# Kernel optimization log

Hardware: AMD Instinct MI355X
Metric: run time of the kernel (lower is better)

The kernel has to match this reference:

```python
import jax, jax.numpy as jnp
import numpy as np

EPS = 1e-5
NUM_HEADS = 12

def _ln(x, g, b):
    m = jnp.mean(x, -1, keepdims=True)
    v = jnp.var(x, -1, keepdims=True)
    return (x - m) * jax.lax.rsqrt(v + EPS) * g + b

def setup_inputs():
    key = jax.random.key(0)
    ks = jax.random.split(key, 8)
    D, Dh = 768, 3072
    B, T, H, Wd = 8, 8, 14, 14
    def w(k, shape, scale=0.02):
        return jax.random.normal(k, shape, jnp.float32) * scale
    return dict(
        x=jax.random.normal(ks[0], (B, T * H * Wd + 1, D), jnp.float32),
        W_mq=w(ks[1], (D, D)), b_mq=jnp.zeros((D,), jnp.float32),
        W_mk=w(ks[2], (D, D)), b_mk=jnp.zeros((D,), jnp.float32),
        g1=jnp.ones((D,), jnp.float32), be1=jnp.zeros((D,), jnp.float32),
        W_qkv=w(ks[3], (3 * D, D)),
        W_proj=w(ks[4], (D, D)), b_proj=jnp.zeros((D,), jnp.float32),
        g2=jnp.ones((D,), jnp.float32), be2=jnp.zeros((D,), jnp.float32),
        W_fc1=w(ks[5], (Dh, D)), b_fc1=jnp.zeros((Dh,), jnp.float32),
        W_fc2=w(ks[6], (D, Dh)), b_fc2=jnp.zeros((D,), jnp.float32),
        B=B, T=T, H=H, Wd=Wd,
    )

def reference(x, W_mq, b_mq, W_mk, b_mk, g1, be1, W_qkv, W_proj, b_proj,
              g2, be2, W_fc1, b_fc1, W_fc2, b_fc2, B, T, H, Wd):
    D = x.shape[-1]
    nh = NUM_HEADS
    hd = D // nh
    res = x
    # cls token: (B,1,D) -> repeated per frame -> (B*T,1,D)
    cls = jnp.repeat(x[:, :1, :], T, axis=1).reshape(B * T, 1, D)
    # spatial tokens: 'b (h w t) m -> (b t) (h w) m'  (t is fastest-varying)
    xs = x[:, 1:, :].reshape(B, H * Wd, T, D).transpose(0, 2, 1, 3).reshape(B * T, H * Wd, D)
    xt = jnp.concatenate([cls, xs], axis=1)  # (BT, N=197, D)
    # learned QK-gated mask
    qm = xt @ W_mq.T + b_mq
    km = xt @ W_mk.T + b_mk
    lm = jnp.einsum('bnd,bmd->bnm', qm, km)
    lm = lm.at[:, 0, 0].set(100.0)  # force cls->cls gate open
    lm = jax.nn.sigmoid(lm)
    # attention (drop rates are 0; drop_path is identity at inference)
    xn = _ln(xt, g1, be1)
    BT, N = xt.shape[0], xt.shape[1]
    qkv = (xn @ W_qkv.T).reshape(BT, N, 3, nh, hd).transpose(2, 0, 3, 1, 4)
    q, k, v = qkv[0], qkv[1], qkv[2]  # (BT, nh, N, hd)
    attn = jax.nn.softmax(jnp.einsum('bhnd,bhmd->bhnm', q, k) * (hd ** -0.5), axis=-1)
    attn = attn * lm[:, None, :, :]  # gate attention probs with learned mask
    o = jnp.einsum('bhnm,bhmd->bhnd', attn, v).transpose(0, 2, 1, 3).reshape(BT, N, D)
    o = o @ W_proj.T + b_proj
    # gather cls back (mean over frames) and scatter tokens back
    cls_o = jnp.mean(o[:, 0, :].reshape(B, T, D), axis=1, keepdims=True)  # (B,1,D)
    xs_o = o[:, 1:, :].reshape(B, T, H * Wd, D).transpose(0, 2, 1, 3).reshape(B, H * Wd * T, D)
    y = res + jnp.concatenate([cls_o, xs_o], axis=1)
    # MLP
    h = _ln(y, g2, be2)
    h = jax.nn.gelu(h @ W_fc1.T + b_fc1, approximate=False)
    y = y + (h @ W_fc2.T + b_fc2)
    return (y, lm)
```

## Files before the change

### kernel.cpp

```cpp
#include <hip/hip_runtime.h>
#include <cstdint>

typedef _Float16 f16;
typedef f16 f16x2 __attribute__((ext_vector_type(2)));
typedef f16 f16x4 __attribute__((ext_vector_type(4)));
typedef f16 f16x8 __attribute__((ext_vector_type(8)));
typedef float f32x4 __attribute__((ext_vector_type(4)));

constexpr int D = 768;
constexpr int NTOK = 197;
constexpr int BT = 64;
constexpr int ROWS_A = BT * NTOK;
constexpr int SEQ = 1569;
constexpr int ROWS_Y = 8 * SEQ;
constexpr int DH = 3072;
constexpr int CW = 2304;
constexpr long Y_ELEMS = (long)ROWS_Y * D;

__device__ __forceinline__ void gload_lds16(const f16* g, f16* l) {
  __builtin_amdgcn_global_load_lds(
      (const __attribute__((address_space(1))) void*)g,
      (__attribute__((address_space(3))) void*)l, 16, 0, 0);
}

__global__ __launch_bounds__(256) void cvt_f16(const float* __restrict__ in,
                                               f16* __restrict__ out, int n4) {
  int i = blockIdx.x * 256 + threadIdx.x;
  if (i >= n4) return;
  const float4 v = *(const float4*)(in + (size_t)i * 4);
  f16x4 o = {(f16)v.x, (f16)v.y, (f16)v.z, (f16)v.w};
  *(f16x4*)(out + (size_t)i * 4) = o;
}

__global__ __launch_bounds__(256) void concat2_f32(const float* __restrict__ a,
                                                   const float* __restrict__ b,
                                                   float* __restrict__ o, int n) {
  int i = blockIdx.x * 256 + threadIdx.x;
  if (i < n) o[i] = a[i];
  else if (i < 2 * n) o[i] = b[i - n];
}

__global__ __launch_bounds__(192) void build_xt_xn(
    const float* __restrict__ x, const float* __restrict__ g1,
    const float* __restrict__ be1, f16* __restrict__ xt, f16* __restrict__ xn) {
  const int rid = blockIdx.x;
  const int bt = rid / NTOK, n = rid % NTOK;
  const int b = bt >> 3, t = bt & 7;
  const int src = (n == 0) ? b * SEQ : b * SEQ + 1 + (n - 1) * 8 + t;
  const int tid = threadIdx.x, d0 = tid * 4;
  const float4 v = *(const float4*)(x + (size_t)src * D + d0);
  float s = v.x + v.y + v.z + v.w;
  float q = v.x * v.x + v.y * v.y + v.z * v.z + v.w * v.w;
  const int lane = tid & 63, wv = tid >> 6;
  for (int off = 32; off; off >>= 1) {
    s += __shfl_xor(s, off);
    q += __shfl_xor(q, off);
  }
  __shared__ float red[2][3];
  if (lane == 0) { red[0][wv] = s; red[1][wv] = q; }
  __syncthreads();
  s = red[0][0] + red[0][1] + red[0][2];
  q = red[1][0] + red[1][1] + red[1][2];
  const float mean = s * (1.f / 768.f);
  const float var = q * (1.f / 768.f) - mean * mean;
  const float rs = rsqrtf(var + 1e-5f);
  const size_t ob = (size_t)rid * D + d0;
  f16x4 xo = {(f16)v.x, (f16)v.y, (f16)v.z, (f16)v.w};
  *(f16x4*)(xt + ob) = xo;
  const float4 gv = *(const float4*)(g1 + d0);
  const float4 bv = *(const float4*)(be1 + d0);
  f16x4 no = {(f16)((v.x - mean) * rs * gv.x + bv.x),
              (f16)((v.y - mean) * rs * gv.y + bv.y),
              (f16)((v.z - mean) * rs * gv.z + bv.z),
              (f16)((v.w - mean) * rs * gv.w + bv.w)};
  *(f16x4*)(xn + ob) = no;
}

constexpr int EPI_F16 = 0;
constexpr int EPI_F16_BIAS = 1;
constexpr int EPI_SIG = 2;
constexpr int EPI_F16_BIAS_GELU = 3;
constexpr int EPI_F32_BIAS_RES = 4;

template <int EPI>
__global__ __launch_bounds__(256, 3) void gemm_f16(
    const f16* __restrict__ A, const f16* __restrict__ B,
    const float* __restrict__ bias, float* __restrict__ Cf,
    f16* __restrict__ Ch, const float* __restrict__ Res, int M, int N, int K,
    int lda, int ldb, int ldc, long sA, long sB, long sC) {
  constexpr int BM = 128, BN = 128, BK = 32;
  __shared__ f16 As[2][BM][BK];
  __shared__ f16 Bs[2][BN][BK];
  const int tid = threadIdx.x;
  const int bm = blockIdx.y * BM, bn = blockIdx.x * BN;
  const int z = blockIdx.z;
  A += (size_t)z * sA;
  B += (size_t)z * sB;
  const int lane = tid & 63, wave = tid >> 6;
  const int wm = (wave >> 1) * 64, wn = (wave & 1) * 64;
  const int l15 = lane & 15, quad = lane >> 4;

  const int gr = lane >> 2;
  const int gc = (lane & 3) * 8;
  int a_row0 = bm + wave * 16 + gr;       if (a_row0 >= M) a_row0 = M - 1;
  int a_row1 = bm + (wave + 4) * 16 + gr; if (a_row1 >= M) a_row1 = M - 1;
  int b_row0 = bn + wave * 16 + gr;       if (b_row0 >= N) b_row0 = N - 1;
  int b_row1 = bn + (wave + 4) * 16 + gr; if (b_row1 >= N) b_row1 = N - 1;
  const f16* ap0 = A + (size_t)a_row0 * lda + gc;
  const f16* ap1 = A + (size_t)a_row1 * lda + gc;
  const f16* bp0 = B + (size_t)b_row0 * ldb + gc;
  const f16* bp1 = B + (size_t)b_row1 * ldb + gc;

  f32x4 acc[4][4] = {};

  auto stage = [&](int buf, int k) {
    gload_lds16(ap0 + k, &As[buf][wave * 16][0]);
    gload_lds16(ap1 + k, &As[buf][(wave + 4) * 16][0]);
    gload_lds16(bp0 + k, &Bs[buf][wave * 16][0]);
    gload_lds16(bp1 + k, &Bs[buf][(wave + 4) * 16][0]);
  };
  auto compute = [&](int buf) {
    f16x8 af[4], bf[4];
#pragma unroll
    for (int i = 0; i < 4; i++) {
      af[i] = *(const f16x8*)&As[buf][wm + i * 16 + l15][quad * 8];
      bf[i] = *(const f16x8*)&Bs[buf][wn + i * 16 + l15][quad * 8];
    }
#pragma unroll
    for (int i = 0; i < 4; i++)
#pragma unroll
      for (int j = 0; j < 4; j++)
        acc[i][j] =
            __builtin_amdgcn_mfma_f32_16x16x32_f16(af[i], bf[j], acc[i][j], 0, 0, 0);
  };

  stage(0, 0);
  __syncthreads();
  for (int kt = 0; kt < K; kt += 2 * BK) {
    stage(1, kt + BK);
    compute(0);
    __syncthreads();
    if (kt + 2 * BK < K) stage(0, kt + 2 * BK);
    compute(1);
    __syncthreads();
  }

#pragma unroll
  for (int i = 0; i < 4; i++) {
#pragma unroll
    for (int j = 0; j < 4; j++) {
      const int col = bn + wn + j * 16 + l15;
      if (col >= N) continue;
#pragma unroll
      for (int r = 0; r < 4; r++) {
        const int row = bm + wm + i * 16 + quad * 4 + r;
        if (row >= M) continue;
        float v = acc[i][j][r];
        const size_t ci = (size_t)z * sC + (size_t)row * ldc + col;
        if constexpr (EPI == EPI_F16) {
          Ch[ci] = (f16)v;
        } else if constexpr (EPI == EPI_F16_BIAS) {
          Ch[ci] = (f16)(v + bias[col]);
        } else if constexpr (EPI == EPI_SIG) {
          if (row == 0 && col == 0) v = 100.f;
          Cf[ci] = 1.f / (1.f + __expf(-v));
        } else if constexpr (EPI == EPI_F16_BIAS_GELU) {
          const float u = v + bias[col];
          const float t = u * (0.79788456f + 0.0356774081f * u * u);
          const float e = __expf(2.f * t);
          Ch[ci] = (f16)(u * (e / (e + 1.f)));
        } else if constexpr (EPI == EPI_F32_BIAS_RES) {
          Cf[ci] = v + bias[col] + Res[ci];
        }
      }
    }
  }
}

__global__ __launch_bounds__(256, 2) void attn_kernel(
    const f16* __restrict__ qkv, const float* __restrict__ lm,
    f16* __restrict__ o) {
  __shared__ f16 Ks[208][72];
  __shared__ f16 Vt[64][232];
  __shared__ f16 Ps[4][16][40];
  const int bh = blockIdx.x;
  const int bt = bh / 12, h = bh % 12;
  const int tid = threadIdx.x, lane = tid & 63, w = tid >> 6;
  const int l15 = lane & 15, quad = lane >> 4;
  const size_t base = (size_t)bt * NTOK * CW + (size_t)h * 64;

  for (int idx = tid; idx < 208 * 8; idx += 256) {
    const int r = idx >> 3, c = (idx & 7) * 8;
    f16x8 kv = {};
    if (r < NTOK) kv = *(const f16x8*)(qkv + base + (size_t)r * CW + 768 + c);
    *(f16x8*)&Ks[r][c] = kv;
  }
  for (int cb = 0; cb < 8; cb++) {
    const int r = tid;
    if (r < NTOK) {
      const f16x8 vv = *(const f16x8*)(qkv + base + (size_t)r * CW + 1536 + cb * 8);
#pragma unroll
      for (int j = 0; j < 8; j++) Vt[cb * 8 + j][r] = vv[j];
    }
  }
  for (int idx = tid; idx < 64 * 35; idx += 256) {
    const int d = idx / 35, m = NTOK + idx % 35;
    Vt[d][m] = (f16)0.f;
  }
  __syncthreads();

  for (int nt = w; nt < 13; nt += 4) {
    const int nq = nt * 16 + l15;
    const f16* qrow = qkv + base + (size_t)nq * CW;
    const f16x8 aq0 = *(const f16x8*)(qrow + quad * 8);
    const f16x8 aq1 = *(const f16x8*)(qrow + 32 + quad * 8);
    f32x4 S[13];
#pragma unroll
    for (int t = 0; t < 13; t++) {
      const f16x8 bk0 = *(const f16x8*)&Ks[t * 16 + l15][quad * 8];
      const f16x8 bk1 = *(const f16x8*)&Ks[t * 16 + l15][32 + quad * 8];
      f32x4 s = {};
      s = __builtin_amdgcn_mfma_f32_16x16x32_f16(aq0, bk0, s, 0, 0, 0);
      s = __builtin_amdgcn_mfma_f32_16x16x32_f16(aq1, bk1, s, 0, 0, 0);
      S[t] = s;
    }
    float mx[4] = {-3e38f, -3e38f, -3e38f, -3e38f};
#pragma unroll
    for (int t = 0; t < 13; t++) {
      const int m = t * 16 + l15;
#pragma unroll
      for (int r = 0; r < 4; r++) {
        float v = (m < NTOK) ? S[t][r] * 0.125f : -1e30f;
        S[t][r] = v;
        mx[r] = fmaxf(mx[r], v);
      }
    }
#pragma unroll
    for (int off = 1; off < 16; off <<= 1)
#pragma unroll
      for (int r = 0; r < 4; r++) mx[r] = fmaxf(mx[r], __shfl_xor(mx[r], off));
    float den[4] = {0.f, 0.f, 0.f, 0.f};
#pragma unroll
    for (int t = 0; t < 13; t++)
#pragma unroll
      for (int r = 0; r < 4; r++) {
        const float e = __expf(S[t][r] - mx[r]);
        S[t][r] = e;
        den[r] += e;
      }
#pragma unroll
    for (int off = 1; off < 16; off <<= 1)
#pragma unroll
      for (int r = 0; r < 4; r++) den[r] += __shfl_xor(den[r], off);
    float inv[4];
#pragma unroll
    for (int r = 0; r < 4; r++) inv[r] = 1.f / den[r];
#pragma unroll
    for (int t = 0; t < 13; t++) {
      const int m = t * 16 + l15;
#pragma unroll
      for (int r = 0; r < 4; r++) {
        const int nrow = nt * 16 + quad * 4 + r;
        float g = 0.f;
        if (m < NTOK && nrow < NTOK)
          g = lm[((size_t)bt * NTOK + nrow) * NTOK + m];
        S[t][r] *= inv[r] * g;
      }
    }
    f32x4 O[4] = {};
    for (int c = 0; c < 7; c++) {
      __builtin_amdgcn_wave_barrier();
#pragma unroll
      for (int tt = 0; tt < 2; tt++) {
        const int t = 2 * c + tt;
#pragma unroll
        for (int r = 0; r < 4; r++) {
          const f16 pv = (t < 13) ? (f16)S[t][r] : (f16)0.f;
          Ps[w][quad * 4 + r][tt * 16 + l15] = pv;
        }
      }
      __builtin_amdgcn_wave_barrier();
      const f16x8 ap = *(const f16x8*)&Ps[w][l15][quad * 8];
#pragma unroll
      for (int dt = 0; dt < 4; dt++) {
        const f16x8 bv = *(const f16x8*)&Vt[dt * 16 + l15][c * 32 + quad * 8];
        O[dt] = __builtin_amdgcn_mfma_f32_16x16x32_f16(ap, bv, O[dt], 0, 0, 0);
      }
    }
#pragma unroll
    for (int dt = 0; dt < 4; dt++)
#pragma unroll
      for (int r = 0; r < 4; r++) {
        const int nrow = nt * 16 + quad * 4 + r;
        if (nrow < NTOK)
          o[((size_t)bt * NTOK + nrow) * D + h * 64 + dt * 16 + l15] =
              (f16)O[dt][r];
      }
  }
}

__global__ __launch_bounds__(192) void scatter_y_ln(
    const float* __restrict__ x, const f16* __restrict__ po,
    const float* __restrict__ g2, const float* __restrict__ be2,
    float* __restrict__ y, f16* __restrict__ yn) {
  const int rid = blockIdx.x;
  const int b = rid / SEQ, pos = rid % SEQ;
  const int tid = threadIdx.x, d0 = tid * 4;
  float4 v = *(const float4*)(x + (size_t)rid * D + d0);
  if (pos == 0) {
    float ax = 0, ay = 0, az = 0, aw = 0;
    for (int t = 0; t < 8; t++) {
      const f16x4 p = *(const f16x4*)(po + ((size_t)(b * 8 + t) * NTOK) * D + d0);
      ax += (float)p[0]; ay += (float)p[1]; az += (float)p[2]; aw += (float)p[3];
    }
    v.x += ax * 0.125f; v.y += ay * 0.125f; v.z += az * 0.125f; v.w += aw * 0.125f;
  } else {
    const int hw = (pos - 1) >> 3, t = (pos - 1) & 7;
    const f16x4 p =
        *(const f16x4*)(po + ((size_t)((b * 8 + t) * NTOK + 1 + hw)) * D + d0);
    v.x += (float)p[0]; v.y += (float)p[1]; v.z += (float)p[2]; v.w += (float)p[3];
  }
  *(float4*)(y + (size_t)rid * D + d0) = v;
  float s = v.x + v.y + v.z + v.w;
  float q = v.x * v.x + v.y * v.y + v.z * v.z + v.w * v.w;
  const int lane = tid & 63, wv = tid >> 6;
  for (int off = 32; off; off >>= 1) {
    s += __shfl_xor(s, off);
    q += __shfl_xor(q, off);
  }
  __shared__ float red[2][3];
  if (lane == 0) { red[0][wv] = s; red[1][wv] = q; }
  __syncthreads();
  s = red[0][0] + red[0][1] + red[0][2];
  q = red[1][0] + red[1][1] + red[1][2];
  const float mean = s * (1.f / 768.f);
  const float var = q * (1.f / 768.f) - mean * mean;
  const float rs = rsqrtf(var + 1e-5f);
  const float4 gv = *(const float4*)(g2 + d0);
  const float4 bv = *(const float4*)(be2 + d0);
  f16x4 no = {(f16)((v.x - mean) * rs * gv.x + bv.x),
              (f16)((v.y - mean) * rs * gv.y + bv.y),
              (f16)((v.z - mean) * rs * gv.z + bv.z),
              (f16)((v.w - mean) * rs * gv.w + bv.w)};
  *(f16x4*)(yn + (size_t)rid * D + d0) = no;
}

extern "C" void kernel_launch(void* const* d_in, const int* in_sizes, int n_in,
                              void* d_out, int out_size, void* d_ws,
                              size_t ws_size, hipStream_t stream) {
  const float* x = (const float*)d_in[0];
  const float* W_mq = (const float*)d_in[1];
  const float* b_mq = (const float*)d_in[2];
  const float* W_mk = (const float*)d_in[3];
  const float* b_mk = (const float*)d_in[4];
  const float* g1 = (const float*)d_in[5];
  const float* be1 = (const float*)d_in[6];
  const float* W_qkv = (const float*)d_in[7];
  const float* W_proj = (const float*)d_in[8];
  const float* b_proj = (const float*)d_in[9];
  const float* g2 = (const float*)d_in[10];
  const float* be2 = (const float*)d_in[11];
  const float* W_fc1 = (const float*)d_in[12];
  const float* b_fc1 = (const float*)d_in[13];
  const float* W_fc2 = (const float*)d_in[14];
  const float* b_fc2 = (const float*)d_in[15];

  char* ws = (char*)d_ws;
  size_t off = 0;
  auto alloc = [&](size_t bytes) {
    size_t o = off;
    off = (off + bytes + 255) & ~(size_t)255;
    return o;
  };
  const size_t o_wmqk = alloc((size_t)2 * D * D * 2);
  const size_t o_bmqk = alloc((size_t)2 * D * 4);
  const size_t o_wqkv = alloc((size_t)CW * D * 2);
  const size_t o_wproj = alloc((size_t)D * D * 2);
  const size_t o_wfc1 = alloc((size_t)DH * D * 2);
  const size_t o_wfc2 = alloc((size_t)D * DH * 2);
  const size_t o_xt = alloc((size_t)ROWS_A * D * 2);
  const size_t o_xn = alloc((size_t)ROWS_A * D * 2);
  const size_t o_big = alloc((size_t)ROWS_A * CW * 2);
  const size_t o_po = alloc((size_t)ROWS_A * D * 2);
  const size_t o_qmkm = o_big;
  const size_t o_qkv = o_big;
  const size_t o_o = o_xn;
  const size_t o_yn = o_xt;
  const size_t o_h = o_big;

  f16* wmqk = (f16*)(ws + o_wmqk);
  float* bmqk = (float*)(ws + o_bmqk);
  f16* wqkv = (f16*)(ws + o_wqkv);
  f16* wproj = (f16*)(ws + o_wproj);
  f16* wfc1 = (f16*)(ws + o_wfc1);
  f16* wfc2 = (f16*)(ws + o_wfc2);
  f16* xt = (f16*)(ws + o_xt);
  f16* xn = (f16*)(ws + o_xn);
  f16* qmkm = (f16*)(ws + o_qmkm);
  f16* qkv = (f16*)(ws + o_qkv);
  f16* oatt = (f16*)(ws + o_o);
  f16* po = (f16*)(ws + o_po);
  f16* yn = (f16*)(ws + o_yn);
  f16* h = (f16*)(ws + o_h);

  float* y_out = (float*)d_out;
  float* lm_out = (float*)d_out + Y_ELEMS;

  const dim3 blk(256);
  auto cvt = [&](const float* src, f16* dst, int n) {
    cvt_f16<<<dim3((n / 4 + 255) / 256), blk, 0, stream>>>(src, dst, n / 4);
  };
  cvt(W_mq, wmqk, D * D);
  cvt(W_mk, wmqk + (size_t)D * D, D * D);
  cvt(W_qkv, wqkv, CW * D);
  cvt(W_proj, wproj, D * D);
  cvt(W_fc1, wfc1, DH * D);
  cvt(W_fc2, wfc2, D * DH);
  concat2_f32<<<dim3(6), blk, 0, stream>>>(b_mq, b_mk, bmqk, D);

  build_xt_xn<<<dim3(ROWS_A), dim3(192), 0, stream>>>(x, g1, be1, xt, xn);

  auto grd = [](int N_, int M_, int Z_) {
    return dim3((N_ + 127) / 128, (M_ + 127) / 128, Z_);
  };
  gemm_f16<EPI_F16_BIAS><<<grd(2 * D, ROWS_A, 1), blk, 0, stream>>>(
      xt, wmqk, bmqk, nullptr, qmkm, nullptr, ROWS_A, 2 * D, D, D, D, 2 * D,
      0, 0, 0);
  gemm_f16<EPI_SIG><<<grd(NTOK, NTOK, BT), blk, 0, stream>>>(
      qmkm, qmkm + D, nullptr, lm_out, nullptr, nullptr, NTOK, NTOK, D,
      2 * D, 2 * D, NTOK, (long)NTOK * 2 * D, (long)NTOK * 2 * D,
      (long)NTOK * NTOK);
  gemm_f16<EPI_F16><<<grd(CW, ROWS_A, 1), blk, 0, stream>>>(
      xn, wqkv, nullptr, nullptr, qkv, nullptr, ROWS_A, CW, D, D, D, CW,
      0, 0, 0);
  attn_kernel<<<dim3(BT * 12), blk, 0, stream>>>(qkv, lm_out, oatt);
  gemm_f16<EPI_F16_BIAS><<<grd(D, ROWS_A, 1), blk, 0, stream>>>(
      oatt, wproj, b_proj, nullptr, po, nullptr, ROWS_A, D, D, D, D, D,
      0, 0, 0);
  scatter_y_ln<<<dim3(ROWS_Y), dim3(192), 0, stream>>>(x, po, g2, be2, y_out, yn);
  gemm_f16<EPI_F16_BIAS_GELU><<<grd(DH, ROWS_Y, 1), blk, 0, stream>>>(
      yn, wfc1, b_fc1, nullptr, h, nullptr, ROWS_Y, DH, D, D, D, DH, 0, 0, 0);
  gemm_f16<EPI_F32_BIAS_RES><<<grd(D, ROWS_Y, 1), blk, 0, stream>>>(
      h, wfc2, b_fc2, y_out, nullptr, y_out, ROWS_Y, D, DH, DH, DH, D,
      0, 0, 0);
  (void)in_sizes; (void)n_in; (void)out_size; (void)ws_size;
}
```

Baseline: 666.4 us.

## Triple-buffer GEMM K loop, split-K FC2 with atomics, fuse weight conversions

The GEMM main loop moves from two LDS buffers with two barriers per pair of K tiles to three buffers with one barrier per K tile. A vmcnt wait lets the loads two tiles ahead stay in flight while the current tile is computed. FC2 now runs as a 2-way split-K with atomicAdd into y, which doubles its grid. The fc2 bias is folded into the residual write in scatter_y_ln so the atomic epilogue only adds partial sums. The six weight conversion launches are merged into one. The extra LDS (24KB per block) may lower occupancy, and atomics make the FC2 summation order nondeterministic.

```diff
diff --git a/kernel.cpp b/kernel.cpp
--- a/kernel.cpp
+++ b/kernel.cpp
@@ -23,13 +23,31 @@
       (__attribute__((address_space(3))) void*)l, 16, 0, 0);
 }
 
-__global__ __launch_bounds__(256) void cvt_f16(const float* __restrict__ in,
-                                               f16* __restrict__ out, int n4) {
-  int i = blockIdx.x * 256 + threadIdx.x;
-  if (i >= n4) return;
-  const float4 v = *(const float4*)(in + (size_t)i * 4);
+constexpr int DD4 = D * D / 4;
+constexpr int QKV4 = CW * D / 4;
+constexpr int FC4 = DH * D / 4;
+constexpr int WQ_TOT = 3 * DD4 + QKV4 + 2 * FC4;
+
+__global__ __launch_bounds__(256) void cvt_weights(
+    const float* __restrict__ wmq_f, const float* __restrict__ wmk_f,
+    const float* __restrict__ wqkv_f, const float* __restrict__ wproj_f,
+    const float* __restrict__ wfc1_f, const float* __restrict__ wfc2_f,
+    f16* __restrict__ wmqk, f16* __restrict__ wqkv, f16* __restrict__ wproj,
+    f16* __restrict__ wfc1, f16* __restrict__ wfc2) {
+  const int i = blockIdx.x * 256 + threadIdx.x;
+  const float* src;
+  f16* dst;
+  int j;
+  if (i < DD4) { src = wmq_f; dst = wmqk; j = i; }
+  else if (i < 2 * DD4) { src = wmk_f; dst = wmqk + (size_t)D * D; j = i - DD4; }
+  else if (i < 2 * DD4 + QKV4) { src = wqkv_f; dst = wqkv; j = i - 2 * DD4; }
+  else if (i < 3 * DD4 + QKV4) { src = wproj_f; dst = wproj; j = i - 2 * DD4 - QKV4; }
+  else if (i < 3 * DD4 + QKV4 + FC4) { src = wfc1_f; dst = wfc1; j = i - 3 * DD4 - QKV4; }
+  else if (i < WQ_TOT) { src = wfc2_f; dst = wfc2; j = i - 3 * DD4 - QKV4 - FC4; }
+  else return;
+  const float4 v = *(const float4*)(src + (size_t)j * 4);
   f16x4 o = {(f16)v.x, (f16)v.y, (f16)v.z, (f16)v.w};
-  *(f16x4*)(out + (size_t)i * 4) = o;
+  *(f16x4*)(dst + (size_t)j * 4) = o;
 }
 
 __global__ __launch_bounds__(256) void concat2_f32(const float* __restrict__ a,
@@ -81,6 +99,7 @@
 constexpr int EPI_SIG = 2;
 constexpr int EPI_F16_BIAS_GELU = 3;
 constexpr int EPI_F32_BIAS_RES = 4;
+constexpr int EPI_F32_ATOMIC = 5;
 
 template <int EPI>
 __global__ __launch_bounds__(256, 3) void gemm_f16(
@@ -89,8 +108,8 @@
     f16* __restrict__ Ch, const float* __restrict__ Res, int M, int N, int K,
     int lda, int ldb, int ldc, long sA, long sB, long sC) {
   constexpr int BM = 128, BN = 128, BK = 32;
-  __shared__ f16 As[2][BM][BK];
-  __shared__ f16 Bs[2][BN][BK];
+  __shared__ f16 As[3][BM][BK];
+  __shared__ f16 Bs[3][BN][BK];
   const int tid = threadIdx.x;
   const int bm = blockIdx.y * BM, bn = blockIdx.x * BN;
   const int z = blockIdx.z;
@@ -134,16 +153,22 @@
             __builtin_amdgcn_mfma_f32_16x16x32_f16(af[i], bf[j], acc[i][j], 0, 0, 0);
   };
 
+  const int NT = K / BK;
   stage(0, 0);
-  __syncthreads();
-  for (int kt = 0; kt < K; kt += 2 * BK) {
-    stage(1, kt + BK);
-    compute(0);
-    __syncthreads();
-    if (kt + 2 * BK < K) stage(0, kt + 2 * BK);
-    compute(1);
-    __syncthreads();
-  }
+  stage(1, BK);
+  for (int kt = 0; kt < NT - 1; ++kt) {
+    asm volatile("s_waitcnt vmcnt(4)" ::: "memory");
+    __builtin_amdgcn_sched_barrier(0);
+    __builtin_amdgcn_s_barrier();
+    __builtin_amdgcn_sched_barrier(0);
+    if (kt + 2 < NT) stage((kt + 2) % 3, (kt + 2) * BK);
+    compute(kt % 3);
+  }
+  asm volatile("s_waitcnt vmcnt(0)" ::: "memory");
+  __builtin_amdgcn_sched_barrier(0);
+  __builtin_amdgcn_s_barrier();
+  __builtin_amdgcn_sched_barrier(0);
+  compute((NT - 1) % 3);
 
 #pragma unroll
   for (int i = 0; i < 4; i++) {
@@ -171,6 +196,8 @@
           Ch[ci] = (f16)(u * (e / (e + 1.f)));
         } else if constexpr (EPI == EPI_F32_BIAS_RES) {
           Cf[ci] = v + bias[col] + Res[ci];
+        } else if constexpr (EPI == EPI_F32_ATOMIC) {
+          atomicAdd(Cf + ci, v);
         }
       }
     }
@@ -302,6 +329,7 @@
 __global__ __launch_bounds__(192) void scatter_y_ln(
     const float* __restrict__ x, const f16* __restrict__ po,
     const float* __restrict__ g2, const float* __restrict__ be2,
+    const float* __restrict__ bfc2,
     float* __restrict__ y, f16* __restrict__ yn) {
   const int rid = blockIdx.x;
   const int b = rid / SEQ, pos = rid % SEQ;
@@ -320,7 +348,9 @@
         *(const f16x4*)(po + ((size_t)((b * 8 + t) * NTOK + 1 + hw)) * D + d0);
     v.x += (float)p[0]; v.y += (float)p[1]; v.z += (float)p[2]; v.w += (float)p[3];
   }
-  *(float4*)(y + (size_t)rid * D + d0) = v;
+  const float4 b2 = *(const float4*)(bfc2 + d0);
+  float4 vo = {v.x + b2.x, v.y + b2.y, v.z + b2.z, v.w + b2.w};
+  *(float4*)(y + (size_t)rid * D + d0) = vo;
   float s = v.x + v.y + v.z + v.w;
   float q = v.x * v.x + v.y * v.y + v.z * v.z + v.w * v.w;
   const int lane = tid & 63, wv = tid >> 6;
@@ -407,15 +437,8 @@
   float* lm_out = (float*)d_out + Y_ELEMS;
 
   const dim3 blk(256);
-  auto cvt = [&](const float* src, f16* dst, int n) {
-    cvt_f16<<<dim3((n / 4 + 255) / 256), blk, 0, stream>>>(src, dst, n / 4);
-  };
-  cvt(W_mq, wmqk, D * D);
-  cvt(W_mk, wmqk + (size_t)D * D, D * D);
-  cvt(W_qkv, wqkv, CW * D);
-  cvt(W_proj, wproj, D * D);
-  cvt(W_fc1, wfc1, DH * D);
-  cvt(W_fc2, wfc2, D * DH);
+  cvt_weights<<<dim3((WQ_TOT + 255) / 256), blk, 0, stream>>>(
+      W_mq, W_mk, W_qkv, W_proj, W_fc1, W_fc2, wmqk, wqkv, wproj, wfc1, wfc2);
   concat2_f32<<<dim3(6), blk, 0, stream>>>(b_mq, b_mk, bmqk, D);
 
   build_xt_xn<<<dim3(ROWS_A), dim3(192), 0, stream>>>(x, g1, be1, xt, xn);
@@ -437,11 +460,12 @@
   gemm_f16<EPI_F16_BIAS><<<grd(D, ROWS_A, 1), blk, 0, stream>>>(
       oatt, wproj, b_proj, nullptr, po, nullptr, ROWS_A, D, D, D, D, D,
       0, 0, 0);
-  scatter_y_ln<<<dim3(ROWS_Y), dim3(192), 0, stream>>>(x, po, g2, be2, y_out, yn);
+  scatter_y_ln<<<dim3(ROWS_Y), dim3(192), 0, stream>>>(x, po, g2, be2, b_fc2,
+                                                       y_out, yn);
   gemm_f16<EPI_F16_BIAS_GELU><<<grd(DH, ROWS_Y, 1), blk, 0, stream>>>(
       yn, wfc1, b_fc1, nullptr, h, nullptr, ROWS_Y, DH, D, D, D, DH, 0, 0, 0);
-  gemm_f16<EPI_F32_BIAS_RES><<<grd(D, ROWS_Y, 1), blk, 0, stream>>>(
-      h, wfc2, b_fc2, y_out, nullptr, y_out, ROWS_Y, D, DH, DH, DH, D,
-      0, 0, 0);
+  gemm_f16<EPI_F32_ATOMIC><<<grd(D, ROWS_Y, 2), blk, 0, stream>>>(
+      h, wfc2, nullptr, y_out, nullptr, nullptr, ROWS_Y, D, 1536, DH, DH, D,
+      1536, 1536, 0);
   (void)in_sizes; (void)n_in; (void)out_size; (void)ws_size;
 }
```

Measured after the change: 677.1 us. About the same (+1.6%).

## Merge weight conversions into one launch and use 128x64 tiles for N=768 GEMMs

Applied to the files above, without the earlier changes.

Replaces six separate fp32-to-fp16 weight conversion launches with a single kernel that selects source and destination by index range, cutting launch overhead. The GEMM is templated on N-tile width and occupancy. The proj and fc2 GEMMs (N=768) now use 128x64 tiles with launch bounds allowing 4 blocks per CU, doubling block count so the 256 CUs are filled better. The trade-off is lower per-block arithmetic intensity and more A-tile reloads for those GEMMs.

```diff
diff --git a/kernel.cpp b/kernel.cpp
--- a/kernel.cpp
+++ b/kernel.cpp
@@ -23,13 +23,31 @@
       (__attribute__((address_space(3))) void*)l, 16, 0, 0);
 }
 
-__global__ __launch_bounds__(256) void cvt_f16(const float* __restrict__ in,
-                                               f16* __restrict__ out, int n4) {
-  int i = blockIdx.x * 256 + threadIdx.x;
-  if (i >= n4) return;
-  const float4 v = *(const float4*)(in + (size_t)i * 4);
+constexpr int DD4 = D * D / 4;
+constexpr int QKV4 = CW * D / 4;
+constexpr int FC4 = DH * D / 4;
+constexpr int WQ_TOT = 3 * DD4 + QKV4 + 2 * FC4;
+
+__global__ __launch_bounds__(256) void cvt_weights(
+    const float* __restrict__ wmq_f, const float* __restrict__ wmk_f,
+    const float* __restrict__ wqkv_f, const float* __restrict__ wproj_f,
+    const float* __restrict__ wfc1_f, const float* __restrict__ wfc2_f,
+    f16* __restrict__ wmqk, f16* __restrict__ wqkv, f16* __restrict__ wproj,
+    f16* __restrict__ wfc1, f16* __restrict__ wfc2) {
+  const int i = blockIdx.x * 256 + threadIdx.x;
+  const float* src;
+  f16* dst;
+  int j;
+  if (i < DD4) { src = wmq_f; dst = wmqk; j = i; }
+  else if (i < 2 * DD4) { src = wmk_f; dst = wmqk + (size_t)D * D; j = i - DD4; }
+  else if (i < 2 * DD4 + QKV4) { src = wqkv_f; dst = wqkv; j = i - 2 * DD4; }
+  else if (i < 3 * DD4 + QKV4) { src = wproj_f; dst = wproj; j = i - 2 * DD4 - QKV4; }
+  else if (i < 3 * DD4 + QKV4 + FC4) { src = wfc1_f; dst = wfc1; j = i - 3 * DD4 - QKV4; }
+  else if (i < WQ_TOT) { src = wfc2_f; dst = wfc2; j = i - 3 * DD4 - QKV4 - FC4; }
+  else return;
+  const float4 v = *(const float4*)(src + (size_t)j * 4);
   f16x4 o = {(f16)v.x, (f16)v.y, (f16)v.z, (f16)v.w};
-  *(f16x4*)(out + (size_t)i * 4) = o;
+  *(f16x4*)(dst + (size_t)j * 4) = o;
 }
 
 __global__ __launch_bounds__(256) void concat2_f32(const float* __restrict__ a,
@@ -82,22 +100,23 @@
 constexpr int EPI_F16_BIAS_GELU = 3;
 constexpr int EPI_F32_BIAS_RES = 4;
 
-template <int EPI>
-__global__ __launch_bounds__(256, 3) void gemm_f16(
+template <int EPI, int BNT = 128, int WPE = 3>
+__global__ __launch_bounds__(256, WPE) void gemm_f16(
     const f16* __restrict__ A, const f16* __restrict__ B,
     const float* __restrict__ bias, float* __restrict__ Cf,
     f16* __restrict__ Ch, const float* __restrict__ Res, int M, int N, int K,
     int lda, int ldb, int ldc, long sA, long sB, long sC) {
-  constexpr int BM = 128, BN = 128, BK = 32;
+  constexpr int BM = 128, BK = 32;
+  constexpr int NJ = BNT / 32;
   __shared__ f16 As[2][BM][BK];
-  __shared__ f16 Bs[2][BN][BK];
+  __shared__ f16 Bs[2][BNT][BK];
   const int tid = threadIdx.x;
-  const int bm = blockIdx.y * BM, bn = blockIdx.x * BN;
+  const int bm = blockIdx.y * BM, bn = blockIdx.x * BNT;
   const int z = blockIdx.z;
   A += (size_t)z * sA;
   B += (size_t)z * sB;
   const int lane = tid & 63, wave = tid >> 6;
-  const int wm = (wave >> 1) * 64, wn = (wave & 1) * 64;
+  const int wm = (wave >> 1) * 64, wn = (wave & 1) * (BNT / 2);
   const int l15 = lane & 15, quad = lane >> 4;
 
   const int gr = lane >> 2;
@@ -111,25 +130,27 @@
   const f16* bp0 = B + (size_t)b_row0 * ldb + gc;
   const f16* bp1 = B + (size_t)b_row1 * ldb + gc;
 
-  f32x4 acc[4][4] = {};
+  f32x4 acc[4][NJ] = {};
 
   auto stage = [&](int buf, int k) {
     gload_lds16(ap0 + k, &As[buf][wave * 16][0]);
     gload_lds16(ap1 + k, &As[buf][(wave + 4) * 16][0]);
     gload_lds16(bp0 + k, &Bs[buf][wave * 16][0]);
-    gload_lds16(bp1 + k, &Bs[buf][(wave + 4) * 16][0]);
+    if constexpr (BNT == 128)
+      gload_lds16(bp1 + k, &Bs[buf][(wave + 4) * 16][0]);
   };
   auto compute = [&](int buf) {
-    f16x8 af[4], bf[4];
-#pragma unroll
-    for (int i = 0; i < 4; i++) {
+    f16x8 af[4], bf[NJ];
+#pragma unroll
+    for (int i = 0; i < 4; i++)
       af[i] = *(const f16x8*)&As[buf][wm + i * 16 + l15][quad * 8];
-      bf[i] = *(const f16x8*)&Bs[buf][wn + i * 16 + l15][quad * 8];
-    }
+#pragma unroll
+    for (int j = 0; j < NJ; j++)
+      bf[j] = *(const f16x8*)&Bs[buf][wn + j * 16 + l15][quad * 8];
 #pragma unroll
     for (int i = 0; i < 4; i++)
 #pragma unroll
-      for (int j = 0; j < 4; j++)
+      for (int j = 0; j < NJ; j++)
         acc[i][j] =
             __builtin_amdgcn_mfma_f32_16x16x32_f16(af[i], bf[j], acc[i][j], 0, 0, 0);
   };
@@ -148,7 +169,7 @@
 #pragma unroll
   for (int i = 0; i < 4; i++) {
 #pragma unroll
-    for (int j = 0; j < 4; j++) {
+    for (int j = 0; j < NJ; j++) {
       const int col = bn + wn + j * 16 + l15;
       if (col >= N) continue;
 #pragma unroll
@@ -407,21 +428,17 @@
   float* lm_out = (float*)d_out + Y_ELEMS;
 
   const dim3 blk(256);
-  auto cvt = [&](const float* src, f16* dst, int n) {
-    cvt_f16<<<dim3((n / 4 + 255) / 256), blk, 0, stream>>>(src, dst, n / 4);
-  };
-  cvt(W_mq, wmqk, D * D);
-  cvt(W_mk, wmqk + (size_t)D * D, D * D);
-  cvt(W_qkv, wqkv, CW * D);
-  cvt(W_proj, wproj, D * D);
-  cvt(W_fc1, wfc1, DH * D);
-  cvt(W_fc2, wfc2, D * DH);
+  cvt_weights<<<dim3((WQ_TOT + 255) / 256), blk, 0, stream>>>(
+      W_mq, W_mk, W_qkv, W_proj, W_fc1, W_fc2, wmqk, wqkv, wproj, wfc1, wfc2);
   concat2_f32<<<dim3(6), blk, 0, stream>>>(b_mq, b_mk, bmqk, D);
 
   build_xt_xn<<<dim3(ROWS_A), dim3(192), 0, stream>>>(x, g1, be1, xt, xn);
 
   auto grd = [](int N_, int M_, int Z_) {
     return dim3((N_ + 127) / 128, (M_ + 127) / 128, Z_);
+  };
+  auto grd64 = [](int N_, int M_) {
+    return dim3((N_ + 63) / 64, (M_ + 127) / 128, 1);
   };
   gemm_f16<EPI_F16_BIAS><<<grd(2 * D, ROWS_A, 1), blk, 0, stream>>>(
       xt, wmqk, bmqk, nullptr, qmkm, nullptr, ROWS_A, 2 * D, D, D, D, 2 * D,
@@ -434,13 +451,13 @@
       xn, wqkv, nullptr, nullptr, qkv, nullptr, ROWS_A, CW, D, D, D, CW,
       0, 0, 0);
   attn_kernel<<<dim3(BT * 12), blk, 0, stream>>>(qkv, lm_out, oatt);
-  gemm_f16<EPI_F16_BIAS><<<grd(D, ROWS_A, 1), blk, 0, stream>>>(
+  gemm_f16<EPI_F16_BIAS, 64, 4><<<grd64(D, ROWS_A), blk, 0, stream>>>(
       oatt, wproj, b_proj, nullptr, po, nullptr, ROWS_A, D, D, D, D, D,
       0, 0, 0);
   scatter_y_ln<<<dim3(ROWS_Y), dim3(192), 0, stream>>>(x, po, g2, be2, y_out, yn);
   gemm_f16<EPI_F16_BIAS_GELU><<<grd(DH, ROWS_Y, 1), blk, 0, stream>>>(
       yn, wfc1, b_fc1, nullptr, h, nullptr, ROWS_Y, DH, D, D, D, DH, 0, 0, 0);
-  gemm_f16<EPI_F32_BIAS_RES><<<grd(D, ROWS_Y, 1), blk, 0, stream>>>(
+  gemm_f16<EPI_F32_BIAS_RES, 64, 4><<<grd64(D, ROWS_Y), blk, 0, stream>>>(
       h, wfc2, b_fc2, y_out, nullptr, y_out, ROWS_Y, D, DH, DH, DH, D,
       0, 0, 0);
   (void)in_sizes; (void)n_in; (void)out_size; (void)ws_size;
```

Result: no change. 666.2 us (-0.0%).
